# Kernel optimization log

Hardware: AMD Instinct MI355X
Metric: run time of the kernel (lower is better)

## Reference

```python
import jax, jax.numpy as jnp
import numpy as np

NUM_CLASSES = 80
NUM_ATTRIB = 85
SCORE_THR = 0.05
CONF_THR = 0.005
IOU_THR = 0.45
MAX_DET = 100
PRE_NMS_TOPK = 4096  # top-k pre-filter; greedy NMS over these candidates


def _make_anchors():
    strides = [32, 16, 8]
    base_sizes = [[(116, 90), (156, 198), (373, 326)],
                  [(30, 61), (62, 45), (59, 119)],
                  [(10, 13), (16, 30), (33, 23)]]
    feat_sizes = [(19, 19), (38, 38), (76, 76)]
    anchors, strs = [], []
    for s, bs, (fh, fw) in zip(strides, base_sizes, feat_sizes):
        c = s / 2.0
        base = np.array([[c - 0.5 * w, c - 0.5 * h, c + 0.5 * w, c + 0.5 * h]
                         for (w, h) in bs], np.float32)
        xx = np.tile(np.arange(fw, dtype=np.float32) * s, fh)
        yy = np.repeat(np.arange(fh, dtype=np.float32) * s, fw)
        shifts = np.stack([xx, yy, xx, yy], -1)  # [HW,4]
        a = (shifts[:, None, :] + base[None, :, :]).reshape(-1, 4)  # location-major, anchor-minor
        anchors.append(a)
        strs.append(np.full(a.shape[0], s, np.float32))
    return np.concatenate(anchors), np.concatenate(strs)

_ANCHORS, _STRIDES = _make_anchors()


def _iou_one_to_many(box, boxes):
    tl = jnp.maximum(box[:2], boxes[:, :2])
    br = jnp.minimum(box[2:], boxes[:, 2:])
    inter = jnp.prod(jnp.clip(br - tl, 0.0), axis=-1)
    a1 = jnp.prod(box[2:] - box[:2])
    a2 = jnp.prod(boxes[:, 2:] - boxes[:, :2], axis=-1)
    return inter / (a1 + a2 - inter + 1e-12)


def _per_image(pred):  # pred: [N, 85]
    anchors = jnp.asarray(_ANCHORS)
    strides = jnp.asarray(_STRIDES)
    xy = jax.nn.sigmoid(pred[:, :2])
    obj = jax.nn.sigmoid(pred[:, 4])
    cls = jax.nn.sigmoid(pred[:, 5:])
    # decode_bboxes
    centers = (anchors[:, :2] + anchors[:, 2:]) * 0.5 + (xy - 0.5) * strides[:, None]
    whs = (anchors[:, 2:] - anchors[:, :2]) * 0.5 * jnp.exp(pred[:, 2:4])
    boxes = jnp.concatenate([centers - whs, centers + whs], axis=-1)  # [N,4]
    # conf threshold on objectness + score threshold on raw class score (torch order),
    # then multiply by objectness score factor
    valid = (obj[:, None] >= CONF_THR) & (cls > SCORE_THR)
    scores = jnp.where(valid, cls * obj[:, None], -jnp.inf).reshape(-1)  # [N*C]
    top_s, top_i = jax.lax.top_k(scores, PRE_NMS_TOPK)
    bidx = top_i // NUM_CLASSES
    labels = (top_i % NUM_CLASSES).astype(jnp.int32)
    cboxes = boxes[bidx]  # [K,4]
    finite = jnp.isfinite(top_s)
    max_coord = jnp.max(jnp.where(finite[:, None], cboxes, 0.0))
    off = labels.astype(boxes.dtype) * (max_coord + 1.0)  # per-class offset trick
    nms_boxes = cboxes + off[:, None]

    def body(i, state):
        alive, dets, det_labels = state
        j = jnp.argmax(alive)
        s = alive[j]
        keep = s > 0.0
        det = jnp.where(keep, jnp.concatenate([cboxes[j], s[None]]), 0.0)
        dets = dets.at[i].set(det)
        det_labels = det_labels.at[i].set(jnp.where(keep, labels[j], -1))
        suppress = _iou_one_to_many(nms_boxes[j], nms_boxes) > IOU_THR
        alive = jnp.where(suppress, -jnp.inf, alive).at[j].set(-jnp.inf)
        return alive, dets, det_labels

    dets0 = jnp.zeros((MAX_DET, 5), boxes.dtype)
    lbl0 = jnp.full((MAX_DET,), -1, jnp.int32)
    _, dets, det_labels = jax.lax.fori_loop(0, MAX_DET, body, (top_s, dets0, lbl0))
    return dets, det_labels


def _forward(pred_maps):
    B = pred_maps[0].shape[0]
    flat = [p.transpose(0, 2, 3, 1).reshape(B, -1, NUM_ATTRIB) for p in pred_maps]
    preds = jnp.concatenate(flat, axis=1)  # [B, N, 85]
    return jax.vmap(_per_image)(preds)  # dets [B,100,5], labels [B,100]


def setup_inputs() -> dict:
    key = jax.random.key(0)
    k0, k1, k2 = jax.random.split(key, 3)
    return {
        "pred_map0": jax.random.normal(k0, (16, 255, 19, 19), jnp.float32),
        "pred_map1": jax.random.normal(k1, (16, 255, 38, 38), jnp.float32),
        "pred_map2": jax.random.normal(k2, (16, 255, 76, 76), jnp.float32),
    }


def reference(pred_map0, pred_map1, pred_map2):
    return _forward([pred_map0, pred_map1, pred_map2])
```

## Files before the change

### kernel.cpp

```cpp
#include <hip/hip_runtime.h>
#include <stdint.h>
#include <math.h>

#define CONF_THR   0.005f
#define SCORE_THRf 0.05f
#define IOU_THR    0.45f
#define TOPK       4096
#define MAXDET     100
#define NHIST      8192
#define NIMG       16
#define BCAP       8192
#define NSLICE     27
#define NBLK       (NIMG * NSLICE)
#define LCAP       1024

__constant__ float c_half[3][3][2] = {
  {{58.0f, 45.0f}, {78.0f, 99.0f}, {186.5f, 163.0f}},
  {{15.0f, 30.5f}, {31.0f, 22.5f}, {29.5f, 59.5f}},
  {{5.0f, 6.5f},  {8.0f, 15.0f},  {16.5f, 11.5f}},
};

__device__ __forceinline__ float sigmoidf_(float x) {
  return 1.0f / (1.0f + expf(-x));
}

template <typename F>
__device__ __forceinline__ void enumerate_scores(
    const float* __restrict__ p0, const float* __restrict__ p1,
    const float* __restrict__ p2, int bx, int tid, F&& emit) {
  const int b = bx / NSLICE;
  const int r = bx % NSLICE;
  int mi, a, h0;
  if (r < 18)      { mi = 2; a = r / 6;        h0 = (r % 6) * 1024; }
  else if (r < 24) { mi = 1; a = (r - 18) >> 1; h0 = ((r - 18) & 1) * 1024; }
  else             { mi = 0; a = r - 24;        h0 = 0; }
  const float* p; int HW, nstart;
  if (mi == 2)      { p = p2; HW = 5776; nstart = 5415; }
  else if (mi == 1) { p = p1; HW = 1444; nstart = 1083; }
  else              { p = p0; HW = 361;  nstart = 0; }
  const int hw0 = h0 + tid * 4;
  if (hw0 >= HW) return;
  const float* q = p + (size_t)b * 255 * HW;
  const float* orow = q + (size_t)(a * 85 + 4) * HW;

  float so[4]; bool ov[4] = {false, false, false, false};
  if (mi != 0) {
    float4 o = *(const float4*)(orow + hw0);
    so[0] = sigmoidf_(o.x); so[1] = sigmoidf_(o.y);
    so[2] = sigmoidf_(o.z); so[3] = sigmoidf_(o.w);
    #pragma unroll
    for (int k = 0; k < 4; ++k) ov[k] = so[k] >= CONF_THR;
  } else {
    #pragma unroll
    for (int k = 0; k < 4; ++k)
      if (hw0 + k < HW) { so[k] = sigmoidf_(orow[hw0 + k]); ov[k] = so[k] >= CONF_THR; }
  }

  for (int c = 0; c < 80; ++c) {
    const float* crow = q + (size_t)(a * 85 + 5 + c) * HW;
    float cv[4];
    if (mi != 0) {
      float4 v = *(const float4*)(crow + hw0);
      cv[0] = v.x; cv[1] = v.y; cv[2] = v.z; cv[3] = v.w;
    } else {
      #pragma unroll
      for (int k = 0; k < 4; ++k) cv[k] = (hw0 + k < HW) ? crow[hw0 + k] : -100.0f;
    }
    #pragma unroll
    for (int k = 0; k < 4; ++k) {
      if (!ov[k]) continue;
      float cs = sigmoidf_(cv[k]);
      if (cs > SCORE_THRf) {
        float sc = __fmul_rn(cs, so[k]);
        unsigned bits = __float_as_uint(sc);
        unsigned idx = (unsigned)((nstart + (hw0 + k) * 3 + a) * 80 + c);
        emit(bits, idx);
      }
    }
  }
}

template <bool PRIV>
__global__ void __launch_bounds__(256) k_hist(const float* __restrict__ p0,
                                              const float* __restrict__ p1,
                                              const float* __restrict__ p2,
                                              unsigned* __restrict__ outHist) {
  __shared__ unsigned lh[NHIST];
  for (int i = threadIdx.x; i < NHIST; i += 256) lh[i] = 0;
  __syncthreads();
  enumerate_scores(p0, p1, p2, blockIdx.x, threadIdx.x,
                   [&](unsigned bits, unsigned) { atomicAdd(&lh[bits >> 17], 1u); });
  __syncthreads();
  if (PRIV) {
    unsigned* dst = outHist + (size_t)blockIdx.x * NHIST;
    for (int i = threadIdx.x; i < NHIST; i += 256) dst[i] = lh[i];
  } else {
    unsigned* dst = outHist + (size_t)(blockIdx.x / NSLICE) * NHIST;
    for (int i = threadIdx.x; i < NHIST; i += 256) if (lh[i]) atomicAdd(&dst[i], lh[i]);
  }
}

__global__ void __launch_bounds__(256) k_merge(const unsigned* __restrict__ priv,
                                               unsigned* __restrict__ merged) {
  const int b = blockIdx.y;
  const int u = blockIdx.x * 256 + threadIdx.x;
  const unsigned* base = priv + (size_t)b * NSLICE * NHIST + u;
  unsigned s = 0;
  #pragma unroll
  for (int sl = 0; sl < NSLICE; ++sl) s += base[(size_t)sl * NHIST];
  merged[(size_t)b * NHIST + u] = s;
}

__global__ void k_scan(const unsigned* __restrict__ hist, int* __restrict__ bb1) {
  __shared__ unsigned h[NHIST];
  __shared__ unsigned csum[256];
  const int b = blockIdx.x;
  const unsigned* gh = hist + (size_t)b * NHIST;
  for (int i = threadIdx.x; i < NHIST; i += 256) h[i] = gh[i];
  __syncthreads();
  unsigned s = 0;
  for (int j = 0; j < 32; ++j) s += h[threadIdx.x * 32 + j];
  csum[threadIdx.x] = s;
  __syncthreads();
  if (threadIdx.x == 0) {
    unsigned acc = 0; int found = -1;
    for (int c2 = 255; c2 >= 0; --c2) {
      if (acc + csum[c2] >= TOPK) {
        for (int k2 = c2 * 32 + 31; k2 >= c2 * 32; --k2) {
          if (acc + h[k2] >= TOPK) { found = k2; break; }
          acc += h[k2];
        }
        break;
      } else acc += csum[c2];
    }
    bb1[b] = found;
  }
}

__global__ void __launch_bounds__(256) k_collect(const float* __restrict__ p0,
                                                 const float* __restrict__ p1,
                                                 const float* __restrict__ p2,
                                                 const int* __restrict__ bb1v,
                                                 unsigned* __restrict__ candCount,
                                                 unsigned* __restrict__ bCount,
                                                 unsigned long long* __restrict__ candKeys,
                                                 unsigned long long* __restrict__ blist) {
  __shared__ unsigned long long wbuf[LCAP];
  __shared__ unsigned long long bbuf[LCAP];
  __shared__ unsigned cnt2[2];
  __shared__ unsigned base2[2];
  const int b = blockIdx.x / NSLICE;
  if (threadIdx.x < 2) cnt2[threadIdx.x] = 0;
  __syncthreads();
  const int Bb1 = bb1v[b];
  unsigned long long* ckg = candKeys + (size_t)b * TOPK;
  unsigned long long* blg = blist + (size_t)b * BCAP;

  enumerate_scores(p0, p1, p2, blockIdx.x, threadIdx.x,
    [&](unsigned bits, unsigned idx) {
      int bkt = (int)(bits >> 17);
      if (bkt < Bb1) return;
      unsigned long long key = ((unsigned long long)(bits ^ 0x80000000u) << 32) |
                               (unsigned long long)(0xFFFFFFFFu - idx);
      if (bkt > Bb1) {
        unsigned pos = atomicAdd(&cnt2[0], 1u);
        if (pos < LCAP) wbuf[pos] = key;
        else { unsigned g = atomicAdd(&candCount[b], 1u); if (g < TOPK) ckg[g] = key; }
      } else {
        unsigned pos = atomicAdd(&cnt2[1], 1u);
        if (pos < LCAP) bbuf[pos] = key;
        else { unsigned g = atomicAdd(&bCount[b], 1u); if (g < BCAP) blg[g] = key; }
      }
    });
  __syncthreads();
  unsigned wn = min(cnt2[0], (unsigned)LCAP);
  unsigned bn = min(cnt2[1], (unsigned)LCAP);
  if (threadIdx.x == 0) base2[0] = wn ? atomicAdd(&candCount[b], wn) : 0u;
  if (threadIdx.x == 1) base2[1] = bn ? atomicAdd(&bCount[b], bn) : 0u;
  __syncthreads();
  for (unsigned i = threadIdx.x; i < wn; i += 256) {
    unsigned g = base2[0] + i; if (g < TOPK) ckg[g] = wbuf[i];
  }
  for (unsigned i = threadIdx.x; i < bn; i += 256) {
    unsigned g = base2[1] + i; if (g < BCAP) blg[g] = bbuf[i];
  }
}

__device__ __forceinline__ void bitonic_desc(unsigned long long* sb, int p2, int nthr, int tid) {
  for (int k = 2; k <= p2; k <<= 1) {
    for (int j = k >> 1; j > 0; j >>= 1) {
      for (int i = tid; i < p2; i += nthr) {
        int ixj = i ^ j;
        if (ixj > i) {
          unsigned long long A = sb[i], B2 = sb[ixj];
          bool up = (i & k) == 0;
          if (up ? (A < B2) : (A > B2)) { sb[i] = B2; sb[ixj] = A; }
        }
      }
      __syncthreads();
    }
  }
}

__global__ void __launch_bounds__(1024) k_bsort(const unsigned* __restrict__ candCount,
                                                const unsigned* __restrict__ bCount,
                                                unsigned long long* __restrict__ candKeys,
                                                const unsigned long long* __restrict__ blist) {
  __shared__ unsigned long long sb[BCAP];
  const int b = blockIdx.x;
  unsigned C1 = candCount[b]; if (C1 > TOPK) C1 = TOPK;
  unsigned m = bCount[b];     if (m > BCAP) m = BCAP;
  int need = TOPK - (int)C1;
  int take = need > 0 ? (need < (int)m ? need : (int)m) : 0;
  unsigned long long* ck = candKeys + (size_t)b * TOPK;
  const unsigned long long* bl = blist + (size_t)b * BCAP;
  if (take > 0) {
    int p2 = 1; while (p2 < (int)m) p2 <<= 1;
    for (int i = threadIdx.x; i < p2; i += 1024) sb[i] = (i < (int)m) ? bl[i] : 0ull;
    __syncthreads();
    bitonic_desc(sb, p2, 1024, threadIdx.x);
    for (int i = threadIdx.x; i < take; i += 1024) ck[C1 + i] = sb[i];
  }
  for (int i = (int)C1 + take + threadIdx.x; i < TOPK; i += 1024) ck[i] = 0ull;
}

__global__ void __launch_bounds__(1024) k_csort_decode(
    const float* __restrict__ p0, const float* __restrict__ p1, const float* __restrict__ p2,
    unsigned long long* __restrict__ candKeys, float4* __restrict__ boxS,
    float* __restrict__ maxcv) {
  __shared__ unsigned long long sb[TOPK];
  __shared__ float red[1024];
  const int b = blockIdx.x;
  unsigned long long* ck = candKeys + (size_t)b * TOPK;
  for (int i = threadIdx.x; i < TOPK; i += 1024) sb[i] = ck[i];
  __syncthreads();
  bitonic_desc(sb, TOPK, 1024, threadIdx.x);
  for (int i = threadIdx.x; i < TOPK; i += 1024) ck[i] = sb[i];

  float lmax = -INFINITY;
  float4* bs = boxS + (size_t)b * TOPK;
  for (int i = threadIdx.x; i < TOPK; i += 1024) {
    unsigned long long key = sb[i];
    float4 bx = make_float4(0.f, 0.f, 0.f, 0.f);
    float contrib = 0.0f;
    if (key != 0ull) {
      unsigned idx = 0xFFFFFFFFu - (unsigned)(key & 0xFFFFFFFFull);
      int n = (int)(idx / 80u);
      const float* p; int HW, W, nstart, L; float fs;
      if (n < 1083)      { p = p0; HW = 361;  W = 19; nstart = 0;    fs = 32.f; L = 0; }
      else if (n < 5415) { p = p1; HW = 1444; W = 38; nstart = 1083; fs = 16.f; L = 1; }
      else               { p = p2; HW = 5776; W = 76; nstart = 5415; fs = 8.f;  L = 2; }
      int r = n - nstart; int hw = r / 3; int a = r % 3;
      int gx = hw % W;    int gy = hw / W;
      const float* q = p + (size_t)b * 255 * HW + hw;
      float tx = q[(size_t)(a * 85 + 0) * HW];
      float ty = q[(size_t)(a * 85 + 1) * HW];
      float tw = q[(size_t)(a * 85 + 2) * HW];
      float th = q[(size_t)(a * 85 + 3) * HW];
      float acx = __fadd_rn((float)gx * fs, 0.5f * fs);
      float acy = __fadd_rn((float)gy * fs, 0.5f * fs);
      float sx = sigmoidf_(tx), sy = sigmoidf_(ty);
      float cx = __fadd_rn(acx, __fmul_rn(__fsub_rn(sx, 0.5f), fs));
      float cy = __fadd_rn(acy, __fmul_rn(__fsub_rn(sy, 0.5f), fs));
      float wx = __fmul_rn(c_half[L][a][0], expf(tw));
      float wy = __fmul_rn(c_half[L][a][1], expf(th));
      bx.x = __fsub_rn(cx, wx); bx.y = __fsub_rn(cy, wy);
      bx.z = __fadd_rn(cx, wx); bx.w = __fadd_rn(cy, wy);
      contrib = fmaxf(fmaxf(bx.x, bx.y), fmaxf(bx.z, bx.w));
    }
    bs[i] = bx;
    lmax = fmaxf(lmax, contrib);
  }
  red[threadIdx.x] = lmax;
  __syncthreads();
  for (int s2 = 512; s2 > 0; s2 >>= 1) {
    if (threadIdx.x < s2) red[threadIdx.x] = fmaxf(red[threadIdx.x], red[threadIdx.x + s2]);
    __syncthreads();
  }
  if (threadIdx.x == 0) maxcv[b] = red[0];
}

__global__ void __launch_bounds__(64) k_nms(const unsigned long long* __restrict__ candKeys,
                                            const float4* __restrict__ boxS,
                                            const float* __restrict__ maxcv,
                                            float* __restrict__ out) {
  const int b = blockIdx.x;
  const int lane = threadIdx.x;
  float* dets = out + (size_t)b * (MAXDET * 5);
  float* lbls = out + (size_t)NIMG * MAXDET * 5 + (size_t)b * MAXDET;
  for (int i = lane; i < MAXDET; i += 64) {
    dets[i * 5 + 0] = 0.f; dets[i * 5 + 1] = 0.f; dets[i * 5 + 2] = 0.f;
    dets[i * 5 + 3] = 0.f; dets[i * 5 + 4] = 0.f;
    lbls[i] = -1.0f;
  }
  __syncthreads();
  const float mc1 = __fadd_rn(maxcv[b], 1.0f);
  const unsigned long long* ck = candKeys + (size_t)b * TOPK;
  const float4* bs = boxS + (size_t)b * TOPK;
  float pbx1[2], pby1[2], pbx2[2], pby2[2], parea[2];
  int P = 0;
  bool done = false;
  for (int base = 0; base < TOPK && !done; base += 64) {
    const int e = base + lane;
    unsigned long long key = ck[e];
    float score = -INFINITY; int c = 0;
    float4 bx = bs[e];
    if (key) {
      unsigned mb = (unsigned)(key >> 32);
      score = __uint_as_float(mb ^ 0x80000000u);
      unsigned idx = 0xFFFFFFFFu - (unsigned)(key & 0xFFFFFFFFull);
      c = (int)(idx % 80u);
    }
    float off = __fmul_rn((float)c, mc1);
    float nx1 = __fadd_rn(bx.x, off), ny1 = __fadd_rn(bx.y, off);
    float nx2 = __fadd_rn(bx.z, off), ny2 = __fadd_rn(bx.w, off);
    for (int t = 0; t < 64; ++t) {
      float s_e = __shfl(score, t);
      if (!(s_e > 0.0f)) { done = true; break; }
      float ex1 = __shfl(nx1, t), ey1 = __shfl(ny1, t);
      float ex2 = __shfl(nx2, t), ey2 = __shfl(ny2, t);
      float ea = __fmul_rn(__fsub_rn(ex2, ex1), __fsub_rn(ey2, ey1));
      bool sup = false;
      #pragma unroll
      for (int k2 = 0; k2 < 2; ++k2) {
        int pi = k2 * 64 + lane;
        if (pi < P) {
          float tlx = fmaxf(pbx1[k2], ex1), tly = fmaxf(pby1[k2], ey1);
          float brx = fminf(pbx2[k2], ex2), bry = fminf(pby2[k2], ey2);
          float iw = fmaxf(__fsub_rn(brx, tlx), 0.0f);
          float ih = fmaxf(__fsub_rn(bry, tly), 0.0f);
          float inter = __fmul_rn(iw, ih);
          float denom = __fadd_rn(__fsub_rn(__fadd_rn(parea[k2], ea), inter), 1e-12f);
          float iou = __fdiv_rn(inter, denom);
          if (iou > IOU_THR) sup = true;
        }
      }
      if (!__any(sup)) {
        float cx1 = __shfl(bx.x, t), cy1 = __shfl(bx.y, t);
        float cx2 = __shfl(bx.z, t), cy2 = __shfl(bx.w, t);
        int   ce  = __shfl(c, t);
        if (lane == (P & 63)) {
          int slot = P >> 6;
          pbx1[slot] = ex1; pby1[slot] = ey1; pbx2[slot] = ex2; pby2[slot] = ey2;
          parea[slot] = ea;
        }
        if (lane == 0) {
          dets[P * 5 + 0] = cx1; dets[P * 5 + 1] = cy1;
          dets[P * 5 + 2] = cx2; dets[P * 5 + 3] = cy2;
          dets[P * 5 + 4] = s_e;
          lbls[P] = (float)ce;
        }
        ++P;
        if (P == MAXDET) { done = true; break; }
      }
    }
  }
}

extern "C" void kernel_launch(void* const* d_in, const int* in_sizes, int n_in,
                              void* d_out, int out_size, void* d_ws, size_t ws_size,
                              hipStream_t stream) {
  const float* p0 = (const float*)d_in[0];
  const float* p1 = (const float*)d_in[1];
  const float* p2 = (const float*)d_in[2];
  float* out = (float*)d_out;
  char* ws = (char*)d_ws;

  const size_t OFF_MERGED = 0;
  const size_t OFF_CNT    = 524288;
  const size_t OFF_CK     = 524544;
  const size_t OFF_BL     = 1048832;
  const size_t OFF_BOX    = 2097408;
  const size_t OFF_PRIV   = 3145984;
  const size_t NEED_PRIV  = OFF_PRIV + (size_t)NBLK * NHIST * 4;

  unsigned* merged = (unsigned*)(ws + OFF_MERGED);
  unsigned* candCount = (unsigned*)(ws + OFF_CNT);
  unsigned* bCount = candCount + 16;
  int* bb1 = (int*)(bCount + 16);
  float* maxcv = (float*)(bb1 + 16);
  unsigned long long* candKeys = (unsigned long long*)(ws + OFF_CK);
  unsigned long long* blist = (unsigned long long*)(ws + OFF_BL);
  float4* boxS = (float4*)(ws + OFF_BOX);
  unsigned* priv = (unsigned*)(ws + OFF_PRIV);

  const bool use_priv = ws_size >= NEED_PRIV;
  if (use_priv) {
    hipMemsetAsync(ws + OFF_CNT, 0, 256, stream);
    k_hist<true><<<NBLK, 256, 0, stream>>>(p0, p1, p2, priv);
    k_merge<<<dim3(NHIST / 256, NIMG), 256, 0, stream>>>(priv, merged);
  } else {
    hipMemsetAsync(ws, 0, OFF_CNT + 256, stream);
    k_hist<false><<<NBLK, 256, 0, stream>>>(p0, p1, p2, merged);
  }
  k_scan<<<NIMG, 256, 0, stream>>>(merged, bb1);
  k_collect<<<NBLK, 256, 0, stream>>>(p0, p1, p2, bb1, candCount, bCount, candKeys, blist);
  k_bsort<<<NIMG, 1024, 0, stream>>>(candCount, bCount, candKeys, blist);
  k_csort_decode<<<NIMG, 1024, 0, stream>>>(p0, p1, p2, candKeys, boxS, maxcv);
  k_nms<<<NIMG, 64, 0, stream>>>(candKeys, boxS, maxcv, out);
}
```

Measured before the change: 450.0 us.

## Rework slicing, collect filtering, and fuse register/shuffle bitonic sort with decode

Pixel slices are re-cut into 48 chunks per image, each thread handling 2 pixels, so more blocks run in the histogram and collect passes. In collect, the shared-memory staging buffers are dropped in favour of direct global atomics, and a per-pixel logit threshold derived from the boundary bucket skips the sigmoid for class scores that cannot qualify. The two sort kernels are merged into one that keeps elements in registers and uses shuffles and swizzled shared memory for the bitonic stages, which saves a launch and removes many barriers. Doing every append with a global atomic could raise contention, and the logit threshold uses a small margin that must keep every candidate that qualifies.

New measurement: 1.078 ms. 140% more time.

```diff
diff --git a/kernel.cpp b/kernel.cpp
--- a/kernel.cpp
+++ b/kernel.cpp
@@ -1,6 +1,8 @@
 #include <hip/hip_runtime.h>
 #include <stdint.h>
 #include <math.h>
+
+typedef unsigned long long u64;
 
 #define CONF_THR   0.005f
 #define SCORE_THRf 0.05f
@@ -10,9 +12,9 @@
 #define NHIST      8192
 #define NIMG       16
 #define BCAP       8192
-#define NSLICE     27
+#define CHUNK      512
+#define NSLICE     48
 #define NBLK       (NIMG * NSLICE)
-#define LCAP       1024
 
 __constant__ float c_half[3][3][2] = {
   {{58.0f, 45.0f}, {78.0f, 99.0f}, {186.5f, 163.0f}},
@@ -24,60 +26,22 @@
   return 1.0f / (1.0f + expf(-x));
 }
 
-template <typename F>
-__device__ __forceinline__ void enumerate_scores(
-    const float* __restrict__ p0, const float* __restrict__ p1,
-    const float* __restrict__ p2, int bx, int tid, F&& emit) {
-  const int b = bx / NSLICE;
-  const int r = bx % NSLICE;
-  int mi, a, h0;
-  if (r < 18)      { mi = 2; a = r / 6;        h0 = (r % 6) * 1024; }
-  else if (r < 24) { mi = 1; a = (r - 18) >> 1; h0 = ((r - 18) & 1) * 1024; }
-  else             { mi = 0; a = r - 24;        h0 = 0; }
-  const float* p; int HW, nstart;
-  if (mi == 2)      { p = p2; HW = 5776; nstart = 5415; }
-  else if (mi == 1) { p = p1; HW = 1444; nstart = 1083; }
-  else              { p = p0; HW = 361;  nstart = 0; }
-  const int hw0 = h0 + tid * 4;
-  if (hw0 >= HW) return;
-  const float* q = p + (size_t)b * 255 * HW;
-  const float* orow = q + (size_t)(a * 85 + 4) * HW;
-
-  float so[4]; bool ov[4] = {false, false, false, false};
-  if (mi != 0) {
-    float4 o = *(const float4*)(orow + hw0);
-    so[0] = sigmoidf_(o.x); so[1] = sigmoidf_(o.y);
-    so[2] = sigmoidf_(o.z); so[3] = sigmoidf_(o.w);
-    #pragma unroll
-    for (int k = 0; k < 4; ++k) ov[k] = so[k] >= CONF_THR;
-  } else {
-    #pragma unroll
-    for (int k = 0; k < 4; ++k)
-      if (hw0 + k < HW) { so[k] = sigmoidf_(orow[hw0 + k]); ov[k] = so[k] >= CONF_THR; }
-  }
-
-  for (int c = 0; c < 80; ++c) {
-    const float* crow = q + (size_t)(a * 85 + 5 + c) * HW;
-    float cv[4];
-    if (mi != 0) {
-      float4 v = *(const float4*)(crow + hw0);
-      cv[0] = v.x; cv[1] = v.y; cv[2] = v.z; cv[3] = v.w;
-    } else {
-      #pragma unroll
-      for (int k = 0; k < 4; ++k) cv[k] = (hw0 + k < HW) ? crow[hw0 + k] : -100.0f;
-    }
-    #pragma unroll
-    for (int k = 0; k < 4; ++k) {
-      if (!ov[k]) continue;
-      float cs = sigmoidf_(cv[k]);
-      if (cs > SCORE_THRf) {
-        float sc = __fmul_rn(cs, so[k]);
-        unsigned bits = __float_as_uint(sc);
-        unsigned idx = (unsigned)((nstart + (hw0 + k) * 3 + a) * 80 + c);
-        emit(bits, idx);
-      }
-    }
-  }
+__device__ __forceinline__ bool slice_decode(const float* __restrict__ p0,
+                                             const float* __restrict__ p1,
+                                             const float* __restrict__ p2,
+                                             int bx, int tid,
+                                             int& b, const float*& q, int& HW,
+                                             int& nstart, int& a, int& hw0) {
+  b = bx / NSLICE;
+  int r = bx % NSLICE;
+  const float* p; int ch;
+  if (r < 36)      { p = p2; HW = 5776; nstart = 5415; a = r / 12;      ch = r % 12; }
+  else if (r < 45) { p = p1; HW = 1444; nstart = 1083; a = (r - 36) / 3; ch = (r - 36) % 3; }
+  else             { p = p0; HW = 361;  nstart = 0;    a = r - 45;      ch = 0; }
+  hw0 = ch * CHUNK + tid * 2;
+  if (hw0 >= HW) return false;
+  q = p + (size_t)b * 255 * HW;
+  return true;
 }
 
 template <bool PRIV>
@@ -88,12 +52,40 @@
   __shared__ unsigned lh[NHIST];
   for (int i = threadIdx.x; i < NHIST; i += 256) lh[i] = 0;
   __syncthreads();
-  enumerate_scores(p0, p1, p2, blockIdx.x, threadIdx.x,
-                   [&](unsigned bits, unsigned) { atomicAdd(&lh[bits >> 17], 1u); });
+  int b; const float* q; int HW, nstart, a, hw0;
+  bool act = slice_decode(p0, p1, p2, blockIdx.x, threadIdx.x, b, q, HW, nstart, a, hw0);
+  if (act) {
+    const bool aligned = (HW & 1) == 0;
+    const bool e1 = (hw0 + 1 < HW);
+    const float* orow = q + (size_t)(a * 85 + 4) * HW + hw0;
+    float o0, o1;
+    if (aligned) { float2 ov = *(const float2*)orow; o0 = ov.x; o1 = ov.y; }
+    else { o0 = orow[0]; o1 = e1 ? orow[1] : -100.0f; }
+    float so0 = sigmoidf_(o0), so1 = sigmoidf_(o1);
+    bool ov0 = so0 >= CONF_THR;
+    bool ov1 = e1 && (so1 >= CONF_THR);
+    if (ov0 || ov1) {
+      for (int c = 0; c < 80; ++c) {
+        const float* crow = q + (size_t)(a * 85 + 5 + c) * HW + hw0;
+        float c0, c1;
+        if (aligned) { float2 v = *(const float2*)crow; c0 = v.x; c1 = v.y; }
+        else { c0 = crow[0]; c1 = e1 ? crow[1] : -100.0f; }
+        if (ov0) {
+          float cs = sigmoidf_(c0);
+          if (cs > SCORE_THRf) atomicAdd(&lh[__float_as_uint(__fmul_rn(cs, so0)) >> 17], 1u);
+        }
+        if (ov1) {
+          float cs = sigmoidf_(c1);
+          if (cs > SCORE_THRf) atomicAdd(&lh[__float_as_uint(__fmul_rn(cs, so1)) >> 17], 1u);
+        }
+      }
+    }
+  }
   __syncthreads();
   if (PRIV) {
     unsigned* dst = outHist + (size_t)blockIdx.x * NHIST;
-    for (int i = threadIdx.x; i < NHIST; i += 256) dst[i] = lh[i];
+    for (int i = threadIdx.x * 4; i < NHIST; i += 1024)
+      *(uint4*)(dst + i) = *(const uint4*)(&lh[i]);
   } else {
     unsigned* dst = outHist + (size_t)(blockIdx.x / NSLICE) * NHIST;
     for (int i = threadIdx.x; i < NHIST; i += 256) if (lh[i]) atomicAdd(&dst[i], lh[i]);
@@ -143,104 +135,158 @@
                                                  const int* __restrict__ bb1v,
                                                  unsigned* __restrict__ candCount,
                                                  unsigned* __restrict__ bCount,
-                                                 unsigned long long* __restrict__ candKeys,
-                                                 unsigned long long* __restrict__ blist) {
-  __shared__ unsigned long long wbuf[LCAP];
-  __shared__ unsigned long long bbuf[LCAP];
-  __shared__ unsigned cnt2[2];
-  __shared__ unsigned base2[2];
-  const int b = blockIdx.x / NSLICE;
-  if (threadIdx.x < 2) cnt2[threadIdx.x] = 0;
-  __syncthreads();
+                                                 u64* __restrict__ candKeys,
+                                                 u64* __restrict__ blist) {
+  int b; const float* q; int HW, nstart, a, hw0;
+  if (!slice_decode(p0, p1, p2, blockIdx.x, threadIdx.x, b, q, HW, nstart, a, hw0)) return;
   const int Bb1 = bb1v[b];
-  unsigned long long* ckg = candKeys + (size_t)b * TOPK;
-  unsigned long long* blg = blist + (size_t)b * BCAP;
-
-  enumerate_scores(p0, p1, p2, blockIdx.x, threadIdx.x,
-    [&](unsigned bits, unsigned idx) {
+  const float T = (Bb1 > 0) ? __uint_as_float((unsigned)Bb1 << 17) : 0.0f;
+  const bool aligned = (HW & 1) == 0;
+  const bool e1 = (hw0 + 1 < HW);
+  const float* orow = q + (size_t)(a * 85 + 4) * HW + hw0;
+  float o0, o1;
+  if (aligned) { float2 ov = *(const float2*)orow; o0 = ov.x; o1 = ov.y; }
+  else { o0 = orow[0]; o1 = e1 ? orow[1] : -100.0f; }
+  float so0 = sigmoidf_(o0), so1 = sigmoidf_(o1);
+  bool ov0 = so0 >= CONF_THR;
+  bool ov1 = e1 && (so1 >= CONF_THR);
+  if (!ov0 && !ov1) return;
+  float cth0 = 1e30f, cth1 = 1e30f;
+  if (ov0) {
+    cth0 = -1e30f;
+    if (Bb1 > 0) {
+      float u = __fdiv_rn(T, so0);
+      cth0 = (u >= 1.0f) ? 15.0f : (logf(__fdiv_rn(u, __fsub_rn(1.0f, u))) - 0.05f);
+    }
+  }
+  if (ov1) {
+    cth1 = -1e30f;
+    if (Bb1 > 0) {
+      float u = __fdiv_rn(T, so1);
+      cth1 = (u >= 1.0f) ? 15.0f : (logf(__fdiv_rn(u, __fsub_rn(1.0f, u))) - 0.05f);
+    }
+  }
+  u64* ckg = candKeys + (size_t)b * TOPK;
+  u64* blg = blist + (size_t)b * BCAP;
+  const int n0 = (nstart + hw0 * 3 + a) * 80;
+  const int n1 = n0 + 240;
+  for (int c = 0; c < 80; ++c) {
+    const float* crow = q + (size_t)(a * 85 + 5 + c) * HW + hw0;
+    float c0, c1;
+    if (aligned) { float2 v = *(const float2*)crow; c0 = v.x; c1 = v.y; }
+    else { c0 = crow[0]; c1 = e1 ? crow[1] : -100.0f; }
+    #pragma unroll
+    for (int k = 0; k < 2; ++k) {
+      float cl = k ? c1 : c0;
+      if (cl <= (k ? cth1 : cth0)) continue;
+      float so = k ? so1 : so0;
+      float cs = sigmoidf_(cl);
+      if (cs <= SCORE_THRf) continue;
+      unsigned bits = __float_as_uint(__fmul_rn(cs, so));
       int bkt = (int)(bits >> 17);
-      if (bkt < Bb1) return;
-      unsigned long long key = ((unsigned long long)(bits ^ 0x80000000u) << 32) |
-                               (unsigned long long)(0xFFFFFFFFu - idx);
+      if (bkt < Bb1) continue;
+      unsigned idx = (unsigned)((k ? n1 : n0) + c);
+      u64 key = ((u64)(bits ^ 0x80000000u) << 32) | (u64)(0xFFFFFFFFu - idx);
       if (bkt > Bb1) {
-        unsigned pos = atomicAdd(&cnt2[0], 1u);
-        if (pos < LCAP) wbuf[pos] = key;
-        else { unsigned g = atomicAdd(&candCount[b], 1u); if (g < TOPK) ckg[g] = key; }
+        unsigned g = atomicAdd(&candCount[b], 1u); if (g < TOPK) ckg[g] = key;
       } else {
-        unsigned pos = atomicAdd(&cnt2[1], 1u);
-        if (pos < LCAP) bbuf[pos] = key;
-        else { unsigned g = atomicAdd(&bCount[b], 1u); if (g < BCAP) blg[g] = key; }
+        unsigned g = atomicAdd(&bCount[b], 1u); if (g < BCAP) blg[g] = key;
       }
-    });
-  __syncthreads();
-  unsigned wn = min(cnt2[0], (unsigned)LCAP);
-  unsigned bn = min(cnt2[1], (unsigned)LCAP);
-  if (threadIdx.x == 0) base2[0] = wn ? atomicAdd(&candCount[b], wn) : 0u;
-  if (threadIdx.x == 1) base2[1] = bn ? atomicAdd(&bCount[b], bn) : 0u;
-  __syncthreads();
-  for (unsigned i = threadIdx.x; i < wn; i += 256) {
-    unsigned g = base2[0] + i; if (g < TOPK) ckg[g] = wbuf[i];
-  }
-  for (unsigned i = threadIdx.x; i < bn; i += 256) {
-    unsigned g = base2[1] + i; if (g < BCAP) blg[g] = bbuf[i];
-  }
-}
-
-__device__ __forceinline__ void bitonic_desc(unsigned long long* sb, int p2, int nthr, int tid) {
-  for (int k = 2; k <= p2; k <<= 1) {
+    }
+  }
+}
+
+__device__ __forceinline__ int swz(int i) { return i ^ ((i >> 4) & 0xF); }
+
+__device__ __forceinline__ u64 shflx64(u64 x, int m) {
+  unsigned lo = __shfl_xor((unsigned)x, m);
+  unsigned hi = __shfl_xor((unsigned)(x >> 32), m);
+  return ((u64)hi << 32) | lo;
+}
+
+template <int V>
+__device__ void bitonic_hybrid_desc(u64* sb, u64 (&r)[V], int t) {
+  const int N = 1024 * V;
+  for (int k = 2; k <= N; k <<= 1) {
     for (int j = k >> 1; j > 0; j >>= 1) {
-      for (int i = tid; i < p2; i += nthr) {
-        int ixj = i ^ j;
-        if (ixj > i) {
-          unsigned long long A = sb[i], B2 = sb[ixj];
-          bool up = (i & k) == 0;
-          if (up ? (A < B2) : (A > B2)) { sb[i] = B2; sb[ixj] = A; }
+      if (j >= 64 * V) {
+        __syncthreads();
+        #pragma unroll
+        for (int v = 0; v < V; ++v) sb[swz(t * V + v)] = r[v];
+        __syncthreads();
+        #pragma unroll
+        for (int v = 0; v < V; ++v) {
+          int i = t * V + v;
+          u64 A = r[v], B = sb[swz(i ^ j)];
+          bool up = (i & k) == 0, lower = (i & j) == 0;
+          r[v] = (up == lower) ? (A > B ? A : B) : (A < B ? A : B);
+        }
+      } else if (j >= V) {
+        int d = j / V;
+        #pragma unroll
+        for (int v = 0; v < V; ++v) {
+          int i = t * V + v;
+          u64 A = r[v], B = shflx64(r[v], d);
+          bool up = (i & k) == 0, lower = (i & j) == 0;
+          r[v] = (up == lower) ? (A > B ? A : B) : (A < B ? A : B);
+        }
+      } else {
+        #pragma unroll
+        for (int v = 0; v < V; ++v) {
+          if ((v & j) == 0) {
+            int i = t * V + v;
+            u64 A = r[v], B = r[v ^ j];
+            bool up = (i & k) == 0;
+            u64 mx = A > B ? A : B, mn = A > B ? B : A;
+            r[v] = up ? mx : mn; r[v ^ j] = up ? mn : mx;
+          }
         }
       }
-      __syncthreads();
-    }
-  }
-}
-
-__global__ void __launch_bounds__(1024) k_bsort(const unsigned* __restrict__ candCount,
-                                                const unsigned* __restrict__ bCount,
-                                                unsigned long long* __restrict__ candKeys,
-                                                const unsigned long long* __restrict__ blist) {
-  __shared__ unsigned long long sb[BCAP];
-  const int b = blockIdx.x;
+    }
+  }
+}
+
+__global__ void __launch_bounds__(1024) k_sortdecode(
+    const unsigned* __restrict__ candCount, const unsigned* __restrict__ bCount,
+    u64* __restrict__ candKeys, const u64* __restrict__ blist,
+    const float* __restrict__ p0, const float* __restrict__ p1, const float* __restrict__ p2,
+    float4* __restrict__ boxS, float* __restrict__ maxcv) {
+  __shared__ u64 sb[8192];
+  const int b = blockIdx.x, t = threadIdx.x;
   unsigned C1 = candCount[b]; if (C1 > TOPK) C1 = TOPK;
   unsigned m = bCount[b];     if (m > BCAP) m = BCAP;
   int need = TOPK - (int)C1;
   int take = need > 0 ? (need < (int)m ? need : (int)m) : 0;
-  unsigned long long* ck = candKeys + (size_t)b * TOPK;
-  const unsigned long long* bl = blist + (size_t)b * BCAP;
+  const u64* bl = blist + (size_t)b * BCAP;
+  u64* ck = candKeys + (size_t)b * TOPK;
   if (take > 0) {
-    int p2 = 1; while (p2 < (int)m) p2 <<= 1;
-    for (int i = threadIdx.x; i < p2; i += 1024) sb[i] = (i < (int)m) ? bl[i] : 0ull;
+    u64 r8[8];
+    #pragma unroll
+    for (int v = 0; v < 8; ++v) { int i = t * 8 + v; r8[v] = (i < (int)m) ? bl[i] : 0ull; }
+    bitonic_hybrid_desc<8>(sb, r8, t);
     __syncthreads();
-    bitonic_desc(sb, p2, 1024, threadIdx.x);
-    for (int i = threadIdx.x; i < take; i += 1024) ck[C1 + i] = sb[i];
-  }
-  for (int i = (int)C1 + take + threadIdx.x; i < TOPK; i += 1024) ck[i] = 0ull;
-}
-
-__global__ void __launch_bounds__(1024) k_csort_decode(
-    const float* __restrict__ p0, const float* __restrict__ p1, const float* __restrict__ p2,
-    unsigned long long* __restrict__ candKeys, float4* __restrict__ boxS,
-    float* __restrict__ maxcv) {
-  __shared__ unsigned long long sb[TOPK];
-  __shared__ float red[1024];
-  const int b = blockIdx.x;
-  unsigned long long* ck = candKeys + (size_t)b * TOPK;
-  for (int i = threadIdx.x; i < TOPK; i += 1024) sb[i] = ck[i];
-  __syncthreads();
-  bitonic_desc(sb, TOPK, 1024, threadIdx.x);
-  for (int i = threadIdx.x; i < TOPK; i += 1024) ck[i] = sb[i];
-
+    #pragma unroll
+    for (int v = 0; v < 8; ++v) sb[swz(t * 8 + v)] = r8[v];
+  }
+  __syncthreads();
+  u64 r4[4];
+  #pragma unroll
+  for (int v = 0; v < 4; ++v) {
+    int i = t * 4 + v;
+    u64 key = 0ull;
+    if (i < (int)C1) key = ck[i];
+    else if (i < (int)C1 + take) key = sb[swz(i - (int)C1)];
+    r4[v] = key;
+  }
+  __syncthreads();
+  bitonic_hybrid_desc<4>(sb, r4, t);
   float lmax = -INFINITY;
   float4* bs = boxS + (size_t)b * TOPK;
-  for (int i = threadIdx.x; i < TOPK; i += 1024) {
-    unsigned long long key = sb[i];
+  #pragma unroll
+  for (int v = 0; v < 4; ++v) {
+    int i = t * 4 + v;
+    u64 key = r4[v];
+    ck[i] = key;
     float4 bx = make_float4(0.f, 0.f, 0.f, 0.f);
     float contrib = 0.0f;
     if (key != 0ull) {
@@ -250,20 +296,20 @@
       if (n < 1083)      { p = p0; HW = 361;  W = 19; nstart = 0;    fs = 32.f; L = 0; }
       else if (n < 5415) { p = p1; HW = 1444; W = 38; nstart = 1083; fs = 16.f; L = 1; }
       else               { p = p2; HW = 5776; W = 76; nstart = 5415; fs = 8.f;  L = 2; }
-      int r = n - nstart; int hw = r / 3; int a = r % 3;
+      int r = n - nstart; int hw = r / 3; int an = r % 3;
       int gx = hw % W;    int gy = hw / W;
-      const float* q = p + (size_t)b * 255 * HW + hw;
-      float tx = q[(size_t)(a * 85 + 0) * HW];
-      float ty = q[(size_t)(a * 85 + 1) * HW];
-      float tw = q[(size_t)(a * 85 + 2) * HW];
-      float th = q[(size_t)(a * 85 + 3) * HW];
+      const float* qq = p + (size_t)b * 255 * HW + hw;
+      float tx = qq[(size_t)(an * 85 + 0) * HW];
+      float ty = qq[(size_t)(an * 85 + 1) * HW];
+      float tw = qq[(size_t)(an * 85 + 2) * HW];
+      float th = qq[(size_t)(an * 85 + 3) * HW];
       float acx = __fadd_rn((float)gx * fs, 0.5f * fs);
       float acy = __fadd_rn((float)gy * fs, 0.5f * fs);
       float sx = sigmoidf_(tx), sy = sigmoidf_(ty);
       float cx = __fadd_rn(acx, __fmul_rn(__fsub_rn(sx, 0.5f), fs));
       float cy = __fadd_rn(acy, __fmul_rn(__fsub_rn(sy, 0.5f), fs));
-      float wx = __fmul_rn(c_half[L][a][0], expf(tw));
-      float wy = __fmul_rn(c_half[L][a][1], expf(th));
+      float wx = __fmul_rn(c_half[L][an][0], expf(tw));
+      float wy = __fmul_rn(c_half[L][an][1], expf(th));
       bx.x = __fsub_rn(cx, wx); bx.y = __fsub_rn(cy, wy);
       bx.z = __fadd_rn(cx, wx); bx.w = __fadd_rn(cy, wy);
       contrib = fmaxf(fmaxf(bx.x, bx.y), fmaxf(bx.z, bx.w));
@@ -271,16 +317,17 @@
     bs[i] = bx;
     lmax = fmaxf(lmax, contrib);
   }
-  red[threadIdx.x] = lmax;
-  __syncthreads();
-  for (int s2 = 512; s2 > 0; s2 >>= 1) {
-    if (threadIdx.x < s2) red[threadIdx.x] = fmaxf(red[threadIdx.x], red[threadIdx.x + s2]);
+  float* red = (float*)(sb + 4096);
+  red[t] = lmax;
+  for (int s = 512; s > 0; s >>= 1) {
     __syncthreads();
-  }
-  if (threadIdx.x == 0) maxcv[b] = red[0];
-}
-
-__global__ void __launch_bounds__(64) k_nms(const unsigned long long* __restrict__ candKeys,
+    if (t < s) red[t] = fmaxf(red[t], red[t + s]);
+  }
+  __syncthreads();
+  if (t == 0) maxcv[b] = red[0];
+}
+
+__global__ void __launch_bounds__(64) k_nms(const u64* __restrict__ candKeys,
                                             const float4* __restrict__ boxS,
                                             const float* __restrict__ maxcv,
                                             float* __restrict__ out) {
@@ -293,16 +340,15 @@
     dets[i * 5 + 3] = 0.f; dets[i * 5 + 4] = 0.f;
     lbls[i] = -1.0f;
   }
-  __syncthreads();
   const float mc1 = __fadd_rn(maxcv[b], 1.0f);
-  const unsigned long long* ck = candKeys + (size_t)b * TOPK;
+  const u64* ck = candKeys + (size_t)b * TOPK;
   const float4* bs = boxS + (size_t)b * TOPK;
   float pbx1[2], pby1[2], pbx2[2], pby2[2], parea[2];
   int P = 0;
   bool done = false;
   for (int base = 0; base < TOPK && !done; base += 64) {
     const int e = base + lane;
-    unsigned long long key = ck[e];
+    u64 key = ck[e];
     float score = -INFINITY; int c = 0;
     float4 bx = bs[e];
     if (key) {
@@ -314,11 +360,11 @@
     float off = __fmul_rn((float)c, mc1);
     float nx1 = __fadd_rn(bx.x, off), ny1 = __fadd_rn(bx.y, off);
     float nx2 = __fadd_rn(bx.z, off), ny2 = __fadd_rn(bx.w, off);
-    for (int t = 0; t < 64; ++t) {
-      float s_e = __shfl(score, t);
+    for (int tt = 0; tt < 64; ++tt) {
+      float s_e = __shfl(score, tt);
       if (!(s_e > 0.0f)) { done = true; break; }
-      float ex1 = __shfl(nx1, t), ey1 = __shfl(ny1, t);
-      float ex2 = __shfl(nx2, t), ey2 = __shfl(ny2, t);
+      float ex1 = __shfl(nx1, tt), ey1 = __shfl(ny1, tt);
+      float ex2 = __shfl(nx2, tt), ey2 = __shfl(ny2, tt);
       float ea = __fmul_rn(__fsub_rn(ex2, ex1), __fsub_rn(ey2, ey1));
       bool sup = false;
       #pragma unroll
@@ -336,9 +382,9 @@
         }
       }
       if (!__any(sup)) {
-        float cx1 = __shfl(bx.x, t), cy1 = __shfl(bx.y, t);
-        float cx2 = __shfl(bx.z, t), cy2 = __shfl(bx.w, t);
-        int   ce  = __shfl(c, t);
+        float cx1 = __shfl(bx.x, tt), cy1 = __shfl(bx.y, tt);
+        float cx2 = __shfl(bx.z, tt), cy2 = __shfl(bx.w, tt);
+        int   ce  = __shfl(c, tt);
         if (lane == (P & 63)) {
           int slot = P >> 6;
           pbx1[slot] = ex1; pby1[slot] = ey1; pbx2[slot] = ex2; pby2[slot] = ey2;
@@ -379,8 +425,8 @@
   unsigned* bCount = candCount + 16;
   int* bb1 = (int*)(bCount + 16);
   float* maxcv = (float*)(bb1 + 16);
-  unsigned long long* candKeys = (unsigned long long*)(ws + OFF_CK);
-  unsigned long long* blist = (unsigned long long*)(ws + OFF_BL);
+  u64* candKeys = (u64*)(ws + OFF_CK);
+  u64* blist = (u64*)(ws + OFF_BL);
   float4* boxS = (float4*)(ws + OFF_BOX);
   unsigned* priv = (unsigned*)(ws + OFF_PRIV);
 
@@ -395,7 +441,7 @@
   }
   k_scan<<<NIMG, 256, 0, stream>>>(merged, bb1);
   k_collect<<<NBLK, 256, 0, stream>>>(p0, p1, p2, bb1, candCount, bCount, candKeys, blist);
-  k_bsort<<<NIMG, 1024, 0, stream>>>(candCount, bCount, candKeys, blist);
-  k_csort_decode<<<NIMG, 1024, 0, stream>>>(p0, p1, p2, candKeys, boxS, maxcv);
+  k_sortdecode<<<NIMG, 1024, 0, stream>>>(candCount, bCount, candKeys, blist,
+                                          p0, p1, p2, boxS, maxcv);
   k_nms<<<NIMG, 64, 0, stream>>>(candKeys, boxS, maxcv, out);
 }
```
